# Kernel tuning notes

Measured on AMD Instinct MI355X. Metric: run time of the kernel, lower is better.

Reference implementation:

```python
import jax, jax.numpy as jnp
import numpy as np

N = 100000       # nodes
E = 1600000      # edges (before self loops)
IN = 128
OUT = 128
H = 4            # heads
FH = OUT // H    # per-head dim = 32
EPS = 1e-5
NEG_SLOPE = 0.2  # PyG GATConv leaky_relu slope


def _gat(x, src, dst, W, a_src, a_dst, b):
    """PyG-style GATConv (concat=True, eval-mode dropout)."""
    n = x.shape[0]
    xw = (x @ W).reshape(n, H, FH)                     # [N,H,FH]
    al_s = jnp.einsum('nhf,hf->nh', xw, a_src)         # [N,H]
    al_d = jnp.einsum('nhf,hf->nh', xw, a_dst)
    e = jax.nn.leaky_relu(al_s[src] + al_d[dst], NEG_SLOPE)   # [E',H]
    m = jax.ops.segment_max(e, dst, num_segments=n)           # segment softmax (stable)
    ee = jnp.exp(e - m[dst])
    den = jax.ops.segment_sum(ee, dst, num_segments=n)
    alpha = ee / den[dst]                                      # [E',H]
    out = jax.ops.segment_sum(alpha[:, :, None] * xw[src], dst, num_segments=n)  # [N,H,FH]
    return out.reshape(n, H * FH) + b


def _bn(x, gamma, beta):
    mu = x.mean(0)
    var = x.var(0)
    return gamma * (x - mu) * jax.lax.rsqrt(var + EPS) + beta


def setup_inputs() -> dict:
    key = jax.random.key(0)
    ks = jax.random.split(key, 10)
    x = jax.random.normal(ks[0], (N, IN), jnp.float32)
    edge_index = jax.random.randint(ks[1], (2, E), 0, N, dtype=jnp.int32)
    W1 = jax.random.normal(ks[2], (IN, OUT), jnp.float32) / np.float32(np.sqrt(IN))
    a1_src = jax.random.normal(ks[3], (H, FH), jnp.float32) * 0.1
    a1_dst = jax.random.normal(ks[4], (H, FH), jnp.float32) * 0.1
    b1 = jnp.zeros((OUT,), jnp.float32)
    g1 = jnp.ones((OUT,), jnp.float32)
    beta1 = jnp.zeros((OUT,), jnp.float32)
    W2 = jax.random.normal(ks[5], (OUT, OUT), jnp.float32) / np.float32(np.sqrt(OUT))
    a2_src = jax.random.normal(ks[6], (H, FH), jnp.float32) * 0.1
    a2_dst = jax.random.normal(ks[7], (H, FH), jnp.float32) * 0.1
    b2 = jnp.zeros((OUT,), jnp.float32)
    g2 = jnp.ones((OUT,), jnp.float32)
    beta2 = jnp.zeros((OUT,), jnp.float32)
    return dict(x=x, edge_index=edge_index, W1=W1, a1_src=a1_src, a1_dst=a1_dst, b1=b1,
                g1=g1, beta1=beta1, W2=W2, a2_src=a2_src, a2_dst=a2_dst, b2=b2,
                g2=g2, beta2=beta2)


def reference(x, edge_index, W1, a1_src, a1_dst, b1, g1, beta1,
              W2, a2_src, a2_dst, b2, g2, beta2):
    n = x.shape[0]
    loops = jnp.arange(n, dtype=edge_index.dtype)          # PyG add_self_loops=True
    src = jnp.concatenate([edge_index[0], loops])
    dst = jnp.concatenate([edge_index[1], loops])
    h = jax.nn.elu(_bn(_gat(x, src, dst, W1, a1_src, a1_dst, b1), g1, beta1))
    h = jax.nn.elu(_bn(_gat(h, src, dst, W2, a2_src, a2_dst, b2), g2, beta2))
    return h
```

## Files before the change

### kernel.cpp

```cpp
#include <hip/hip_runtime.h>

#define NF   128
#define NH   4
#define FHD  32
#define BNEPS 1e-5f
#define SLOPE 0.2f

typedef unsigned int uint32;

__device__ __forceinline__ float bf_lo(uint32 u) { return __uint_as_float(u << 16); }
__device__ __forceinline__ float bf_hi(uint32 u) { return __uint_as_float(u & 0xFFFF0000u); }
__device__ __forceinline__ uint32 bf_rnd(float x) {
  uint32 u = __float_as_uint(x);
  return (u + 0x7FFFu + ((u >> 16) & 1u)) >> 16;
}
__device__ __forceinline__ uint32 pack2(float a, float b) {
  return bf_rnd(a) | (bf_rnd(b) << 16);
}

__global__ __launch_bounds__(256) void gemm_xw_al(
    const float* __restrict__ X, const float* __restrict__ W,
    const float* __restrict__ a_src, const float* __restrict__ a_dst,
    uint32* __restrict__ XWB, float* __restrict__ ALs, float* __restrict__ ALd,
    int nrows)
{
  __shared__ __align__(16) float sXT[128][68];
  __shared__ __align__(16) float sW[32][128];
  __shared__ float sAs[128], sAd[128];
  const int t = threadIdx.x;
  const int row0 = blockIdx.x * 64;

  for (int i = t; i < 64 * 32; i += 256) {
    int r = i >> 5, c4 = (i & 31) << 2;
    int gr = row0 + r;
    float4 v = make_float4(0.f, 0.f, 0.f, 0.f);
    if (gr < nrows) v = *(const float4*)&X[(size_t)gr * NF + c4];
    sXT[c4 + 0][r] = v.x; sXT[c4 + 1][r] = v.y;
    sXT[c4 + 2][r] = v.z; sXT[c4 + 3][r] = v.w;
  }
  if (t < 128) sAs[t] = a_src[t];
  else         sAd[t - 128] = a_dst[t - 128];

  const int tx = t & 15;
  const int ty = t >> 4;
  const int c0 = tx << 3;
  const int r0 = ty << 2;
  float acc[4][8];
  #pragma unroll
  for (int i = 0; i < 4; i++)
    #pragma unroll
    for (int j = 0; j < 8; j++) acc[i][j] = 0.f;

  for (int q = 0; q < 4; ++q) {
    __syncthreads();
    for (int i = t; i < 32 * 32; i += 256) {
      int kk = i >> 5, c4 = (i & 31) << 2;
      *(float4*)&sW[kk][c4] = *(const float4*)&W[(size_t)(q * 32 + kk) * NF + c4];
    }
    __syncthreads();
    #pragma unroll 4
    for (int kk = 0; kk < 32; ++kk) {
      int k = q * 32 + kk;
      float4 xv = *(const float4*)&sXT[k][r0];
      float4 w0 = *(const float4*)&sW[kk][c0];
      float4 w1 = *(const float4*)&sW[kk][c0 + 4];
      float xr[4] = {xv.x, xv.y, xv.z, xv.w};
      float wr[8] = {w0.x, w0.y, w0.z, w0.w, w1.x, w1.y, w1.z, w1.w};
      #pragma unroll
      for (int i = 0; i < 4; i++)
        #pragma unroll
        for (int j = 0; j < 8; j++)
          acc[i][j] = fmaf(xr[i], wr[j], acc[i][j]);
    }
  }

  const int hd  = tx >> 2;
  const int off = (tx & 3) << 3;
  #pragma unroll
  for (int i = 0; i < 4; i++) {
    int gr = row0 + r0 + i;
    float ps = 0.f, pd = 0.f;
    #pragma unroll
    for (int j = 0; j < 8; j++) {
      ps += acc[i][j] * sAs[hd * FHD + off + j];
      pd += acc[i][j] * sAd[hd * FHD + off + j];
    }
    ps += __shfl_xor(ps, 1); ps += __shfl_xor(ps, 2);
    pd += __shfl_xor(pd, 1); pd += __shfl_xor(pd, 2);
    if (gr < nrows) {
      uint4 pk;
      pk.x = pack2(acc[i][0], acc[i][1]);
      pk.y = pack2(acc[i][2], acc[i][3]);
      pk.z = pack2(acc[i][4], acc[i][5]);
      pk.w = pack2(acc[i][6], acc[i][7]);
      *(uint4*)&XWB[(size_t)gr * 64 + (c0 >> 1)] = pk;
      if ((t & 3) == 0) {
        ALs[gr * NH + hd] = ps;
        ALd[gr * NH + hd] = pd;
      }
    }
  }
}

__global__ void count_rank_kernel(const int* __restrict__ ei,
                                  int* __restrict__ cnt, int* __restrict__ rank,
                                  int nE)
{
  int e = blockIdx.x * blockDim.x + threadIdx.x;
  if (e < nE) rank[e] = atomicAdd(&cnt[ei[nE + e]], 1);
}

__global__ void scan1(const int* __restrict__ cnt, int* __restrict__ excl,
                      int* __restrict__ blockSums, int n)
{
  __shared__ int s[256];
  int i = blockIdx.x * 256 + threadIdx.x;
  int v = (i < n) ? cnt[i] : 0;
  s[threadIdx.x] = v;
  __syncthreads();
  for (int ofs = 1; ofs < 256; ofs <<= 1) {
    int t = (threadIdx.x >= ofs) ? s[threadIdx.x - ofs] : 0;
    __syncthreads();
    s[threadIdx.x] += t;
    __syncthreads();
  }
  if (i < n) excl[i] = s[threadIdx.x] - v;
  if (threadIdx.x == 255) blockSums[blockIdx.x] = s[255];
}

__global__ void scan2(int* __restrict__ blockSums, int nb)
{
  __shared__ int s[1024];
  int tid = threadIdx.x;
  int v = (tid < nb) ? blockSums[tid] : 0;
  s[tid] = v;
  __syncthreads();
  for (int ofs = 1; ofs < 1024; ofs <<= 1) {
    int t = (tid >= ofs) ? s[tid - ofs] : 0;
    __syncthreads();
    s[tid] += t;
    __syncthreads();
  }
  if (tid < nb) blockSums[tid] = s[tid] - v;
}

__global__ void scan3(const int* __restrict__ excl,
                      const int* __restrict__ blockSums,
                      int* __restrict__ rowptr, int n, int nE)
{
  int i = blockIdx.x * blockDim.x + threadIdx.x;
  if (i < n) rowptr[i] = excl[i] + blockSums[i >> 8];
  if (i == n) rowptr[n] = nE;
}

__global__ void scatter2_kernel(const int* __restrict__ ei,
                                const int* __restrict__ rowptr,
                                const int* __restrict__ rank,
                                int* __restrict__ adj, int nE)
{
  int e = blockIdx.x * blockDim.x + threadIdx.x;
  if (e >= nE) return;
  int dst = ei[nE + e];
  adj[rowptr[dst] + rank[e]] = ei[e];
}

__global__ __launch_bounds__(256) void gat_gather_stats(
    const int* __restrict__ rowptr, const int* __restrict__ adj,
    const uint32* __restrict__ xwb,
    const float* __restrict__ ALs, const float* __restrict__ ALd,
    const float* __restrict__ bias,
    float* __restrict__ y, float* __restrict__ stats, int nN)
{
  __shared__ float sst[256];
  sst[threadIdx.x] = 0.f;
  __syncthreads();

  const int lane = threadIdx.x & 63;
  const int wly  = threadIdx.x >> 6;
  const int h    = lane >> 4;
  const int f0   = lane * 2;
  const float b0 = bias[f0], b1 = bias[f0 + 1];
  const int nw   = gridDim.x * 4;

  float s1a = 0.f, s1b = 0.f, s2a = 0.f, s2b = 0.f;

  for (int nd = blockIdx.x * 4 + wly; nd < nN; nd += nw) {
    int node = __builtin_amdgcn_readfirstlane(nd);
    float ad = ALd[node * NH + h];

    float acc0, acc1, den;
    {
      float e = ALs[node * NH + h] + ad;
      e = (e >= 0.f) ? e : SLOPE * e;
      float w = __expf(e);
      uint32 u = xwb[(size_t)node * 64 + lane];
      acc0 = w * bf_lo(u); acc1 = w * bf_hi(u); den = w;
    }

    int beg = rowptr[node];
    int end = rowptr[node + 1];
    int p = beg;
    for (; p + 1 < end; p += 2) {
      int s0 = adj[p], s1 = adj[p + 1];
      uint32 u0 = xwb[(size_t)s0 * 64 + lane];
      uint32 u1 = xwb[(size_t)s1 * 64 + lane];
      float e0 = ALs[s0 * NH + h] + ad; e0 = (e0 >= 0.f) ? e0 : SLOPE * e0;
      float e1 = ALs[s1 * NH + h] + ad; e1 = (e1 >= 0.f) ? e1 : SLOPE * e1;
      float w0 = __expf(e0), w1 = __expf(e1);
      acc0 = fmaf(w0, bf_lo(u0), acc0); acc1 = fmaf(w0, bf_hi(u0), acc1); den += w0;
      acc0 = fmaf(w1, bf_lo(u1), acc0); acc1 = fmaf(w1, bf_hi(u1), acc1); den += w1;
    }
    if (p < end) {
      int s0 = adj[p];
      uint32 u0 = xwb[(size_t)s0 * 64 + lane];
      float e0 = ALs[s0 * NH + h] + ad; e0 = (e0 >= 0.f) ? e0 : SLOPE * e0;
      float w0 = __expf(e0);
      acc0 = fmaf(w0, bf_lo(u0), acc0); acc1 = fmaf(w0, bf_hi(u0), acc1); den += w0;
    }

    float inv = 1.f / den;
    float ox = acc0 * inv + b0;
    float oy = acc1 * inv + b1;
    *(float2*)&y[(size_t)node * NF + f0] = make_float2(ox, oy);
    s1a += ox; s1b += oy;
    s2a += ox * ox; s2b += oy * oy;
  }

  atomicAdd(&sst[f0], s1a);       atomicAdd(&sst[f0 + 1], s1b);
  atomicAdd(&sst[128 + f0], s2a); atomicAdd(&sst[128 + f0 + 1], s2b);
  __syncthreads();
  atomicAdd(&stats[threadIdx.x], sst[threadIdx.x]);
}

__global__ void bn_elu(const float* __restrict__ y,
                       const float* __restrict__ stats,
                       const float* __restrict__ gamma,
                       const float* __restrict__ beta,
                       float* __restrict__ out, int nN)
{
  int t = blockIdx.x * blockDim.x + threadIdx.x;
  int total = nN * NF;
  if (t >= total) return;
  int f = t & (NF - 1);
  float inv_n = 1.f / (float)nN;
  float mu = stats[f] * inv_n;
  float var = stats[NF + f] * inv_n - mu * mu;
  float v = (y[t] - mu) * rsqrtf(var + BNEPS) * gamma[f] + beta[f];
  out[t] = (v > 0.f) ? v : expm1f(v);
}

extern "C" void kernel_launch(void* const* d_in, const int* in_sizes, int n_in,
                              void* d_out, int out_size, void* d_ws, size_t ws_size,
                              hipStream_t stream)
{
  const float* x   = (const float*)d_in[0];
  const int*   ei  = (const int*)d_in[1];
  const float* W1  = (const float*)d_in[2];
  const float* a1s = (const float*)d_in[3];
  const float* a1d = (const float*)d_in[4];
  const float* b1  = (const float*)d_in[5];
  const float* g1  = (const float*)d_in[6];
  const float* be1 = (const float*)d_in[7];
  const float* W2  = (const float*)d_in[8];
  const float* a2s = (const float*)d_in[9];
  const float* a2d = (const float*)d_in[10];
  const float* b2  = (const float*)d_in[11];
  const float* g2  = (const float*)d_in[12];
  const float* be2 = (const float*)d_in[13];
  float* out = (float*)d_out;

  const int nN = in_sizes[0] / NF;
  const int nE = in_sizes[1] / 2;
  const int nb = (nN + 255) / 256;

  float* ws = (float*)d_ws;
  size_t off = 0;
  uint32* xwb  = (uint32*)(ws + off); off += (size_t)nN * 64;
  float* ybuf  = ws + off; off += (size_t)nN * NF;
  float* ALs   = ws + off; off += (size_t)nN * NH;
  float* ALd   = ws + off; off += (size_t)nN * NH;
  float* stats = ws + off; off += 256;
  int* ibase   = (int*)(ws + off);
  int* cnt       = ibase;
  int* excl      = ibase + nN;
  int* blockSums = ibase + 2 * nN;
  int* rowptr    = ibase + 2 * nN + 1024;
  int* rank      = rowptr + nN + 2;
  int* adj       = rank + nE;
  float* hbuf  = out;

  const int gemm_grid = (nN + 63) / 64;
  const int e_grid    = (nE + 255) / 256;
  const int g_grid    = 2048;
  const int bn_grid   = (nN * NF + 255) / 256;

  hipMemsetAsync(cnt, 0, (size_t)nN * sizeof(int), stream);
  count_rank_kernel<<<e_grid, 256, 0, stream>>>(ei, cnt, rank, nE);
  scan1<<<nb, 256, 0, stream>>>(cnt, excl, blockSums, nN);
  scan2<<<1, 1024, 0, stream>>>(blockSums, nb);
  scan3<<<(nN + 256) / 256, 256, 0, stream>>>(excl, blockSums, rowptr, nN, nE);
  scatter2_kernel<<<e_grid, 256, 0, stream>>>(ei, rowptr, rank, adj, nE);

  hipMemsetAsync(stats, 0, 256 * sizeof(float), stream);
  gemm_xw_al<<<gemm_grid, 256, 0, stream>>>(x, W1, a1s, a1d, xwb, ALs, ALd, nN);
  gat_gather_stats<<<g_grid, 256, 0, stream>>>(rowptr, adj, xwb, ALs, ALd, b1,
                                               ybuf, stats, nN);
  bn_elu<<<bn_grid, 256, 0, stream>>>(ybuf, stats, g1, be1, hbuf, nN);

  hipMemsetAsync(stats, 0, 256 * sizeof(float), stream);
  gemm_xw_al<<<gemm_grid, 256, 0, stream>>>(hbuf, W2, a2s, a2d, xwb, ALs, ALd, nN);
  gat_gather_stats<<<g_grid, 256, 0, stream>>>(rowptr, adj, xwb, ALs, ALd, b2,
                                               ybuf, stats, nN);
  bn_elu<<<bn_grid, 256, 0, stream>>>(ybuf, stats, g2, be2, out, nN);
}
```

Baseline: 635.1 us.

## Fuse layer-1 BN+ELU into second GEMM load, unroll gather by four

```diff
diff --git a/kernel.cpp b/kernel.cpp
--- a/kernel.cpp
+++ b/kernel.cpp
@@ -17,29 +17,52 @@
 __device__ __forceinline__ uint32 pack2(float a, float b) {
   return bf_rnd(a) | (bf_rnd(b) << 16);
 }
+__device__ __forceinline__ float elu1(float v) {
+  return (v > 0.f) ? v : expm1f(v);
+}
 
 __global__ __launch_bounds__(256) void gemm_xw_al(
     const float* __restrict__ X, const float* __restrict__ W,
     const float* __restrict__ a_src, const float* __restrict__ a_dst,
+    const float* __restrict__ bn_stats, const float* __restrict__ gamma,
+    const float* __restrict__ beta,
     uint32* __restrict__ XWB, float* __restrict__ ALs, float* __restrict__ ALd,
     int nrows)
 {
   __shared__ __align__(16) float sXT[128][68];
   __shared__ __align__(16) float sW[32][128];
   __shared__ float sAs[128], sAd[128];
+  __shared__ float sScale[128], sShift[128];
   const int t = threadIdx.x;
   const int row0 = blockIdx.x * 64;
+
+  if (t < 128) sAs[t] = a_src[t];
+  else         sAd[t - 128] = a_dst[t - 128];
+  const bool do_bn = (bn_stats != nullptr);
+  if (do_bn && t < 128) {
+    float inv_n = 1.f / (float)nrows;
+    float mu  = bn_stats[t] * inv_n;
+    float var = bn_stats[128 + t] * inv_n - mu * mu;
+    float sc  = gamma[t] * rsqrtf(var + BNEPS);
+    sScale[t] = sc;
+    sShift[t] = beta[t] - mu * sc;
+  }
+  __syncthreads();
 
   for (int i = t; i < 64 * 32; i += 256) {
     int r = i >> 5, c4 = (i & 31) << 2;
     int gr = row0 + r;
     float4 v = make_float4(0.f, 0.f, 0.f, 0.f);
     if (gr < nrows) v = *(const float4*)&X[(size_t)gr * NF + c4];
+    if (do_bn) {
+      v.x = elu1(v.x * sScale[c4 + 0] + sShift[c4 + 0]);
+      v.y = elu1(v.y * sScale[c4 + 1] + sShift[c4 + 1]);
+      v.z = elu1(v.z * sScale[c4 + 2] + sShift[c4 + 2]);
+      v.w = elu1(v.w * sScale[c4 + 3] + sShift[c4 + 3]);
+    }
     sXT[c4 + 0][r] = v.x; sXT[c4 + 1][r] = v.y;
     sXT[c4 + 2][r] = v.z; sXT[c4 + 3][r] = v.w;
   }
-  if (t < 128) sAs[t] = a_src[t];
-  else         sAd[t - 128] = a_dst[t - 128];
 
   const int tx = t & 15;
   const int ty = t >> 4;
@@ -146,11 +169,13 @@
 
 __global__ void scan3(const int* __restrict__ excl,
                       const int* __restrict__ blockSums,
-                      int* __restrict__ rowptr, int n, int nE)
+                      int* __restrict__ rowptr, float* __restrict__ statsz,
+                      int n, int nE)
 {
   int i = blockIdx.x * blockDim.x + threadIdx.x;
   if (i < n) rowptr[i] = excl[i] + blockSums[i >> 8];
   if (i == n) rowptr[n] = nE;
+  if (i < 512) statsz[i] = 0.f;
 }
 
 __global__ void scatter2_kernel(const int* __restrict__ ei,
@@ -200,17 +225,23 @@
     int beg = rowptr[node];
     int end = rowptr[node + 1];
     int p = beg;
-    for (; p + 1 < end; p += 2) {
-      int s0 = adj[p], s1 = adj[p + 1];
+    for (; p + 3 < end; p += 4) {
+      int s0 = adj[p], s1 = adj[p + 1], s2 = adj[p + 2], s3 = adj[p + 3];
       uint32 u0 = xwb[(size_t)s0 * 64 + lane];
       uint32 u1 = xwb[(size_t)s1 * 64 + lane];
+      uint32 u2 = xwb[(size_t)s2 * 64 + lane];
+      uint32 u3 = xwb[(size_t)s3 * 64 + lane];
       float e0 = ALs[s0 * NH + h] + ad; e0 = (e0 >= 0.f) ? e0 : SLOPE * e0;
       float e1 = ALs[s1 * NH + h] + ad; e1 = (e1 >= 0.f) ? e1 : SLOPE * e1;
-      float w0 = __expf(e0), w1 = __expf(e1);
+      float e2 = ALs[s2 * NH + h] + ad; e2 = (e2 >= 0.f) ? e2 : SLOPE * e2;
+      float e3 = ALs[s3 * NH + h] + ad; e3 = (e3 >= 0.f) ? e3 : SLOPE * e3;
+      float w0 = __expf(e0), w1 = __expf(e1), w2 = __expf(e2), w3 = __expf(e3);
       acc0 = fmaf(w0, bf_lo(u0), acc0); acc1 = fmaf(w0, bf_hi(u0), acc1); den += w0;
       acc0 = fmaf(w1, bf_lo(u1), acc0); acc1 = fmaf(w1, bf_hi(u1), acc1); den += w1;
-    }
-    if (p < end) {
+      acc0 = fmaf(w2, bf_lo(u2), acc0); acc1 = fmaf(w2, bf_hi(u2), acc1); den += w2;
+      acc0 = fmaf(w3, bf_lo(u3), acc0); acc1 = fmaf(w3, bf_hi(u3), acc1); den += w3;
+    }
+    for (; p < end; ++p) {
       int s0 = adj[p];
       uint32 u0 = xwb[(size_t)s0 * 64 + lane];
       float e0 = ALs[s0 * NH + h] + ad; e0 = (e0 >= 0.f) ? e0 : SLOPE * e0;
@@ -279,7 +310,9 @@
   float* ybuf  = ws + off; off += (size_t)nN * NF;
   float* ALs   = ws + off; off += (size_t)nN * NH;
   float* ALd   = ws + off; off += (size_t)nN * NH;
-  float* stats = ws + off; off += 256;
+  float* stats = ws + off; off += 512;
+  float* stats1 = stats;
+  float* stats2 = stats + 256;
   int* ibase   = (int*)(ws + off);
   int* cnt       = ibase;
   int* excl      = ibase + nN;
@@ -287,7 +320,6 @@
   int* rowptr    = ibase + 2 * nN + 1024;
   int* rank      = rowptr + nN + 2;
   int* adj       = rank + nE;
-  float* hbuf  = out;
 
   const int gemm_grid = (nN + 63) / 64;
   const int e_grid    = (nE + 255) / 256;
@@ -298,18 +330,19 @@
   count_rank_kernel<<<e_grid, 256, 0, stream>>>(ei, cnt, rank, nE);
   scan1<<<nb, 256, 0, stream>>>(cnt, excl, blockSums, nN);
   scan2<<<1, 1024, 0, stream>>>(blockSums, nb);
-  scan3<<<(nN + 256) / 256, 256, 0, stream>>>(excl, blockSums, rowptr, nN, nE);
+  scan3<<<(nN + 256) / 256, 256, 0, stream>>>(excl, blockSums, rowptr, stats, nN, nE);
   scatter2_kernel<<<e_grid, 256, 0, stream>>>(ei, rowptr, rank, adj, nE);
 
-  hipMemsetAsync(stats, 0, 256 * sizeof(float), stream);
-  gemm_xw_al<<<gemm_grid, 256, 0, stream>>>(x, W1, a1s, a1d, xwb, ALs, ALd, nN);
+  gemm_xw_al<<<gemm_grid, 256, 0, stream>>>(x, W1, a1s, a1d,
+                                            nullptr, nullptr, nullptr,
+                                            xwb, ALs, ALd, nN);
   gat_gather_stats<<<g_grid, 256, 0, stream>>>(rowptr, adj, xwb, ALs, ALd, b1,
-                                               ybuf, stats, nN);
-  bn_elu<<<bn_grid, 256, 0, stream>>>(ybuf, stats, g1, be1, hbuf, nN);
-
-  hipMemsetAsync(stats, 0, 256 * sizeof(float), stream);
-  gemm_xw_al<<<gemm_grid, 256, 0, stream>>>(hbuf, W2, a2s, a2d, xwb, ALs, ALd, nN);
+                                               ybuf, stats1, nN);
+
+  gemm_xw_al<<<gemm_grid, 256, 0, stream>>>(ybuf, W2, a2s, a2d,
+                                            stats1, g1, be1,
+                                            xwb, ALs, ALd, nN);
   gat_gather_stats<<<g_grid, 256, 0, stream>>>(rowptr, adj, xwb, ALs, ALd, b2,
-                                               ybuf, stats, nN);
-  bn_elu<<<bn_grid, 256, 0, stream>>>(ybuf, stats, g2, be2, out, nN);
-}
+                                               ybuf, stats2, nN);
+  bn_elu<<<bn_grid, 256, 0, stream>>>(ybuf, stats2, g2, be2, out, nN);
+}
```

After: 609.2 us. -4.1%, faster.
